# Kernel tuning notes

Hardware: AMD Instinct MI355X
Metric: run time of the kernel (lower is better)

Reference implementation:

```python
import jax, jax.numpy as jnp
import numpy as np
from jax import lax

V = 23       # vocab size (prime -> all nonzero scales invertible mod V)
H = 256      # hidden width of the strictly-causal masked layer
B, L = 512, 1024
TEMP = 1.0

_a = np.arange(V)
# one_hot_minus: out[k] = sum_a x[a] * shift[(a - k) % V]
MINUS_IDX = jnp.asarray((_a[None, :] - _a[:, None]) % V)  # [k, a] -> index into shift
# one_hot_multiply: T[s, k, a] = 1 if (s * a) % V == k
MUL_T = jnp.asarray(np.equal.outer(np.outer(_a, _a) % V, _a).transpose(0, 2, 1).astype(np.float32))  # [s, k, a]
# multiplicative inverse mod V (Fermat: s^(V-2) mod V for prime V); inv(0) := 0
_inv = np.array([pow(int(s), V - 2, V) if s else 0 for s in range(V)])
INV_P = jnp.asarray((_inv[:, None] == _a[None, :]).astype(np.float32))  # [s, k]


def one_hot_argmax(x, temp):
    """Straight-through one-hot argmax (soft = softmax(x/temp))."""
    soft = jax.nn.softmax(x / temp, axis=-1)
    hard = jax.nn.one_hot(jnp.argmax(x, axis=-1), V, dtype=x.dtype)
    return soft + lax.stop_gradient(hard - soft)


def one_hot_minus(x, shift):
    # (x - shift) % V in one-hot space: out[k] = sum_a x[a] * shift[(a-k)%V]
    return jnp.einsum('ba,bka->bk', x, shift[:, MINUS_IDX])


def one_hot_multiply(x, scale):
    # (x * scale) % V in one-hot space
    return jnp.einsum('bs,ba,ska->bk', scale, x, MUL_T)


def setup_inputs() -> dict:
    key = jax.random.key(0)
    k1, k2, k3 = jax.random.split(key, 3)
    x_tokens = jax.random.randint(k1, (B, L), 0, V, dtype=jnp.int32)
    W1 = jax.random.normal(k2, (V, H), jnp.float32) * 0.1
    b1 = jnp.zeros((H,), jnp.float32)
    W2 = jax.random.normal(k3, (H, 2 * V), jnp.float32) * 0.1
    b2 = jnp.zeros((2 * V,), jnp.float32)
    return {"x_tokens": x_tokens, "W1": W1, "b1": b1, "W2": W2, "b2": b2}


def reference(x_tokens, W1, b1, W2, b2):
    x = jax.nn.one_hot(x_tokens, V, dtype=jnp.float32)  # [B, L, V] one-hot inputs

    def step(acc, x_t):
        # acc [B, V] = sum of previously generated one-hot outputs y[0..t-1];
        # this is exactly what the strictly-causal layer sees at position t,
        # so net_t equals layer(padded_inputs)[:, t, :] of the original loop.
        net = jax.nn.relu(acc @ W1 + b1) @ W2 + b2      # [B, 2V]
        loc = one_hot_argmax(net[:, :V], TEMP)
        scale = one_hot_argmax(net[:, V:], TEMP)
        inv_scale = scale @ INV_P                        # one-hot modular inverse
        out_t = one_hot_multiply(one_hot_minus(x_t, loc), inv_scale)
        return acc + out_t, out_t

    acc0 = jnp.zeros((x.shape[0], V), x.dtype)
    _, ys = lax.scan(step, acc0, jnp.swapaxes(x, 0, 1))  # scan over length
    return jnp.swapaxes(ys, 0, 1)                        # [B, L, V]
```

## Files before the change

### kernel.cpp

```cpp
#include <hip/hip_runtime.h>
#include <math.h>

#define V 23
#define HH 256
#define BB 512
#define LL 1024
#define NOUT 46

constexpr unsigned long long packInv(int lo) {
    const int inv[23] = {0,1,12,8,6,14,4,10,3,18,7,21,2,16,5,20,13,19,9,17,15,11,22};
    unsigned long long t = 0;
    for (int i = 0; i < 12; ++i) {
        int idx = lo + i;
        if (idx < 23) t |= (unsigned long long)inv[idx] << (5 * i);
    }
    return t;
}
constexpr unsigned long long INV_T0 = packInv(0);
constexpr unsigned long long INV_T1 = packInv(12);

#define DPPMAX(v, ctrl, rmask)                                                  \
    do {                                                                        \
        unsigned _t = (unsigned)__builtin_amdgcn_update_dpp(                    \
            (int)(v), (int)(v), (ctrl), (rmask), 0xF, false);                   \
        (v) = ((v) > _t) ? (v) : _t;                                            \
    } while (0)

__global__ __launch_bounds__(256, 2)
void daf_kernel(const int* __restrict__ xtok,
                const float* __restrict__ W1,
                const float* __restrict__ b1,
                const float* __restrict__ W2,
                const float* __restrict__ b2,
                float* __restrict__ out)
{
    __shared__ float sW1[V * HH];
    __shared__ float sW2T[NOUT * HH];
    __shared__ float sV[HH];
    __shared__ float sP[2][4][64];
    __shared__ unsigned char sTokB[LL];
    __shared__ unsigned char sKB[LL];

    const int tid = threadIdx.x;
    const int w   = tid >> 6;
    const int l   = tid & 63;
    const int b   = blockIdx.x;

    for (int i = tid; i < V * HH; i += 256) sW1[i] = W1[i];
    for (int i = tid; i < NOUT * HH; i += 256) {
        const int col = i >> 8, row = i & 255;
        sW2T[i] = W2[row * NOUT + col];
    }
    for (int i = tid; i < LL; i += 256) sTokB[i] = (unsigned char)xtok[(size_t)b * LL + i];

    const bool activeA = (l < V);
    const bool activeB = (l >= 32 && l < 32 + V);
    const bool active  = activeA || activeB;
    const int  col     = activeA ? l : (activeB ? (l - 32 + V) : 0);

    double h_pre = (double)b1[tid];
    const float bias = active ? b2[col] : 0.f;

    __syncthreads();

    float4 wr[16];
    {
        const float4* src = (const float4*)&sW2T[col * HH + 64 * w];
        #pragma unroll
        for (int q = 0; q < 16; ++q) wr[q] = src[q];
    }
    __syncthreads();

    for (int t = 0; t < LL; ++t) {
        const int tok = (int)sTokB[t];

        float v = fmaxf((float)h_pre, 0.f);
        sV[tid] = v;

        const float4* pv = (const float4*)(sV + 64 * w);
        float a0 = 0.f, a1 = 0.f, a2 = 0.f, a3 = 0.f;
        #pragma unroll
        for (int q = 0; q < 16; ++q) {
            float4 vv = pv[q];
            a0 = fmaf(vv.x, wr[q].x, a0);
            a1 = fmaf(vv.y, wr[q].y, a1);
            a2 = fmaf(vv.z, wr[q].z, a2);
            a3 = fmaf(vv.w, wr[q].w, a3);
        }
        const int p = t & 1;
        sP[p][w][l] = (a0 + a1) + (a2 + a3);
        __syncthreads();

        float s0 = sP[p][0][l], s1 = sP[p][1][l];
        float s2 = sP[p][2][l], s3 = sP[p][3][l];
        float net = bias + ((s0 + s1) + (s2 + s3));

        int ib = __float_as_int(net);
        unsigned monoraw = (ib < 0) ? ~(unsigned)ib : ((unsigned)ib ^ 0x80000000u);
        const unsigned orig = active ? monoraw : 0u;

        unsigned red = orig;
        DPPMAX(red, 0xB1,  0xF);
        DPPMAX(red, 0x4E,  0xF);
        DPPMAX(red, 0x141, 0xF);
        DPPMAX(red, 0x140, 0xF);
        DPPMAX(red, 0x142, 0xA);
        const unsigned sA = (unsigned)__builtin_amdgcn_readlane((int)red, 16);
        const unsigned sB = (unsigned)__builtin_amdgcn_readlane((int)red, 48);

        const unsigned cmpv = (l < 32) ? sA : sB;
        const unsigned long long bal = __ballot(orig == cmpv);
        const int loc = __builtin_ctzll(bal & 0xFFFFFFFFull);
        const int sc  = __builtin_ctzll(bal >> 32);

        const unsigned long long tt = (sc < 12) ? INV_T0 : INV_T1;
        const int sh  = 5 * (sc - ((sc >= 12) ? 12 : 0));
        const int inv = (int)((tt >> sh) & 31);

        int m = tok - loc;
        m += (m >> 31) & V;
        const int k = (m * inv) % V;

        h_pre += (double)sW1[k * HH + tid];
        if (tid == 0) sKB[t] = (unsigned char)k;
    }

    __syncthreads();
    float* outb = out + (size_t)b * LL * V;
    for (int t = tid; t < LL; t += 256)
        outb[t * V + (int)sKB[t]] = 1.0f;
}

extern "C" void kernel_launch(void* const* d_in, const int* in_sizes, int n_in,
                              void* d_out, int out_size, void* d_ws, size_t ws_size,
                              hipStream_t stream) {
    const int*   xtok = (const int*)d_in[0];
    const float* W1   = (const float*)d_in[1];
    const float* b1   = (const float*)d_in[2];
    const float* W2   = (const float*)d_in[3];
    const float* b2   = (const float*)d_in[4];
    float* out = (float*)d_out;

    hipMemsetAsync(out, 0, (size_t)out_size * sizeof(float), stream);
    daf_kernel<<<BB, 256, 0, stream>>>(xtok, W1, b1, W2, b2, out);
}
```

Measured before the change: 792.5 us.

## Halve block to two waves and broadcast hidden activations via readlane

```diff
diff --git a/kernel.cpp b/kernel.cpp
--- a/kernel.cpp
+++ b/kernel.cpp
@@ -26,7 +26,7 @@
         (v) = ((v) > _t) ? (v) : _t;                                            \
     } while (0)
 
-__global__ __launch_bounds__(256, 2)
+__global__ __launch_bounds__(128, 2)
 void daf_kernel(const int* __restrict__ xtok,
                 const float* __restrict__ W1,
                 const float* __restrict__ b1,
@@ -36,8 +36,7 @@
 {
     __shared__ float sW1[V * HH];
     __shared__ float sW2T[NOUT * HH];
-    __shared__ float sV[HH];
-    __shared__ float sP[2][4][64];
+    __shared__ float sP[2][2][64];
     __shared__ unsigned char sTokB[LL];
     __shared__ unsigned char sKB[LL];
 
@@ -46,54 +45,73 @@
     const int l   = tid & 63;
     const int b   = blockIdx.x;
 
-    for (int i = tid; i < V * HH; i += 256) sW1[i] = W1[i];
-    for (int i = tid; i < NOUT * HH; i += 256) {
+    for (int i = tid; i < V * HH; i += 128) sW1[i] = W1[i];
+    for (int i = tid; i < NOUT * HH; i += 128) {
         const int col = i >> 8, row = i & 255;
         sW2T[i] = W2[row * NOUT + col];
     }
-    for (int i = tid; i < LL; i += 256) sTokB[i] = (unsigned char)xtok[(size_t)b * LL + i];
+    for (int i = tid; i < LL; i += 128) sTokB[i] = (unsigned char)xtok[(size_t)b * LL + i];
 
     const bool activeA = (l < V);
     const bool activeB = (l >= 32 && l < 32 + V);
     const bool active  = activeA || activeB;
     const int  col     = activeA ? l : (activeB ? (l - 32 + V) : 0);
 
-    double h_pre = (double)b1[tid];
+    double h0 = (double)b1[128 * w + l];
+    double h1 = (double)b1[128 * w + 64 + l];
     const float bias = active ? b2[col] : 0.f;
 
     __syncthreads();
 
-    float4 wr[16];
+    float4 wr[32];
     {
-        const float4* src = (const float4*)&sW2T[col * HH + 64 * w];
+        const float4* src = (const float4*)&sW2T[col * HH + 128 * w];
         #pragma unroll
-        for (int q = 0; q < 16; ++q) wr[q] = src[q];
+        for (int q = 0; q < 32; ++q) wr[q] = src[q];
     }
     __syncthreads();
 
     for (int t = 0; t < LL; ++t) {
         const int tok = (int)sTokB[t];
 
-        float v = fmaxf((float)h_pre, 0.f);
-        sV[tid] = v;
+        const float v0f = fmaxf((float)h0, 0.f);
+        const float v1f = fmaxf((float)h1, 0.f);
+        const int vb0 = __float_as_int(v0f);
+        const int vb1 = __float_as_int(v1f);
 
-        const float4* pv = (const float4*)(sV + 64 * w);
         float a0 = 0.f, a1 = 0.f, a2 = 0.f, a3 = 0.f;
         #pragma unroll
         for (int q = 0; q < 16; ++q) {
-            float4 vv = pv[q];
-            a0 = fmaf(vv.x, wr[q].x, a0);
-            a1 = fmaf(vv.y, wr[q].y, a1);
-            a2 = fmaf(vv.z, wr[q].z, a2);
-            a3 = fmaf(vv.w, wr[q].w, a3);
+            const float x0 = __int_as_float(__builtin_amdgcn_readlane(vb0, 4 * q + 0));
+            const float x1 = __int_as_float(__builtin_amdgcn_readlane(vb0, 4 * q + 1));
+            const float x2 = __int_as_float(__builtin_amdgcn_readlane(vb0, 4 * q + 2));
+            const float x3 = __int_as_float(__builtin_amdgcn_readlane(vb0, 4 * q + 3));
+            a0 = fmaf(x0, wr[q].x, a0);
+            a1 = fmaf(x1, wr[q].y, a1);
+            a2 = fmaf(x2, wr[q].z, a2);
+            a3 = fmaf(x3, wr[q].w, a3);
         }
+        #pragma unroll
+        for (int q = 16; q < 32; ++q) {
+            const float x0 = __int_as_float(__builtin_amdgcn_readlane(vb1, 4 * (q - 16) + 0));
+            const float x1 = __int_as_float(__builtin_amdgcn_readlane(vb1, 4 * (q - 16) + 1));
+            const float x2 = __int_as_float(__builtin_amdgcn_readlane(vb1, 4 * (q - 16) + 2));
+            const float x3 = __int_as_float(__builtin_amdgcn_readlane(vb1, 4 * (q - 16) + 3));
+            a0 = fmaf(x0, wr[q].x, a0);
+            a1 = fmaf(x1, wr[q].y, a1);
+            a2 = fmaf(x2, wr[q].z, a2);
+            a3 = fmaf(x3, wr[q].w, a3);
+        }
+        const float mine = (a0 + a1) + (a2 + a3);
+
         const int p = t & 1;
-        sP[p][w][l] = (a0 + a1) + (a2 + a3);
+        sP[p][w][l] = mine;
         __syncthreads();
 
-        float s0 = sP[p][0][l], s1 = sP[p][1][l];
-        float s2 = sP[p][2][l], s3 = sP[p][3][l];
-        float net = bias + ((s0 + s1) + (s2 + s3));
+        const float other = sP[p][1 - w][l];
+        const float pw0 = (w == 0) ? mine : other;
+        const float pw1 = (w == 0) ? other : mine;
+        float net = bias + (pw0 + pw1);
 
         int ib = __float_as_int(net);
         unsigned monoraw = (ib < 0) ? ~(unsigned)ib : ((unsigned)ib ^ 0x80000000u);
@@ -121,13 +139,14 @@
         m += (m >> 31) & V;
         const int k = (m * inv) % V;
 
-        h_pre += (double)sW1[k * HH + tid];
+        h0 += (double)sW1[k * HH + 128 * w + l];
+        h1 += (double)sW1[k * HH + 128 * w + 64 + l];
         if (tid == 0) sKB[t] = (unsigned char)k;
     }
 
     __syncthreads();
     float* outb = out + (size_t)b * LL * V;
-    for (int t = tid; t < LL; t += 256)
+    for (int t = tid; t < LL; t += 128)
         outb[t * V + (int)sKB[t]] = 1.0f;
 }
 
@@ -142,5 +161,5 @@
     float* out = (float*)d_out;
 
     hipMemsetAsync(out, 0, (size_t)out_size * sizeof(float), stream);
-    daf_kernel<<<BB, 256, 0, stream>>>(xtok, W1, b1, W2, b2, out);
+    daf_kernel<<<BB, 128, 0, stream>>>(xtok, W1, b1, W2, b2, out);
 }
```

New measurement: 809.7 us. 2.2% more time.
